# Kernel optimization log

Hardware: AMD Instinct MI355X
Metric: run time of the kernel (lower is better)

The kernel has to match this reference:

```python
import jax, jax.numpy as jnp
import numpy as np
import math

D_MODEL = 256
D_STATE = 64
B, L = 16, 4096
OUT_DIM = 2 * D_MODEL  # bidirectional


def s4d_kernel(log_dt, log_A_real, A_imag, C, L):
    # dt: [d], A: [d, n], C: [d, n, 2]
    dt = jnp.exp(log_dt)
    Cc = C[..., 0] + 1j * C[..., 1]
    A = -jnp.exp(log_A_real) + 1j * A_imag
    dtA = A * dt[:, None]                                   # [d, n]
    Cc = Cc * (jnp.exp(dtA) - 1.0) / (A + 1e-8)
    vand = jnp.exp(dtA[:, :, None] * jnp.arange(L))          # [d, n, L] complex
    K = 2.0 * jnp.einsum('dn,dnl->dl', Cc, vand).real        # [d, L]
    return K


def fft_conv(u, k, L):
    # u: [B, d, L], k: [d, L]; causal conv via zero-padded FFT
    kf = jnp.fft.rfft(k, n=2 * L)
    uf = jnp.fft.rfft(u, n=2 * L)
    return jnp.fft.irfft(uf * kf, n=2 * L)[..., :L]


def setup_inputs() -> dict:
    key = jax.random.key(0)
    ks = jax.random.split(key, 8)
    n = D_STATE // 2

    def kernel_params(k):
        log_dt = jnp.linspace(math.log(0.001), math.log(0.1), D_MODEL)
        log_A_real = jnp.tile(jnp.log(jnp.linspace(0.1, 0.9, n)), (D_MODEL, 1))
        A_imag = jnp.tile(jnp.linspace(0.0, math.pi, n), (D_MODEL, 1))
        C = jax.random.normal(k, (D_MODEL, n, 2)) / math.sqrt(D_STATE)
        return log_dt, log_A_real, A_imag, C

    log_dt_fw, log_A_real_fw, A_imag_fw, C_fw = kernel_params(ks[0])
    log_dt_bw, log_A_real_bw, A_imag_bw, C_bw = kernel_params(ks[1])

    return {
        'x': jax.random.normal(ks[2], (B, L, D_MODEL), dtype=jnp.float32),
        'log_dt_fw': log_dt_fw, 'log_A_real_fw': log_A_real_fw,
        'A_imag_fw': A_imag_fw, 'C_fw': C_fw,
        'log_dt_bw': log_dt_bw, 'log_A_real_bw': log_A_real_bw,
        'A_imag_bw': A_imag_bw, 'C_bw': C_bw,
        'Dskip': jax.random.normal(ks[3], (D_MODEL,)) * 0.01,
        'conv_w': jax.random.normal(ks[4], (2 * OUT_DIM, OUT_DIM)) / math.sqrt(OUT_DIM),
        'conv_b': jnp.zeros((2 * OUT_DIM,)),
        'ln_gamma': jnp.ones((OUT_DIM,)),
        'ln_beta': jnp.zeros((OUT_DIM,)),
    }


def reference(x, log_dt_fw, log_A_real_fw, A_imag_fw, C_fw,
              log_dt_bw, log_A_real_bw, A_imag_bw, C_bw,
              Dskip, conv_w, conv_b, ln_gamma, ln_beta):
    Bsz, Ln, H = x.shape
    u = jnp.swapaxes(x, 1, 2)                                # [B, H, L]

    k_fw = s4d_kernel(log_dt_fw, log_A_real_fw, A_imag_fw, C_fw, Ln)
    y_fw = fft_conv(u, k_fw, Ln) + u * Dskip[:, None]

    u_bw = jnp.flip(u, axis=-1)
    k_bw = s4d_kernel(log_dt_bw, log_A_real_bw, A_imag_bw, C_bw, Ln)
    y_bw = fft_conv(u_bw, k_bw, Ln) + u_bw * Dskip[:, None]
    y_bw = jnp.flip(y_bw, axis=-1)

    y = jnp.concatenate([y_fw, y_bw], axis=1)                # [B, 2H, L]
    y = jax.nn.gelu(y, approximate=False)
    # pointwise conv1d (kernel_size=1): channels 2H -> 4H
    y = jnp.einsum('oc,bcl->bol', conv_w, y) + conv_b[None, :, None]
    a, b = jnp.split(y, 2, axis=1)                           # GLU over channel dim
    y = a * jax.nn.sigmoid(b)                                # [B, 2H, L]
    y = jnp.swapaxes(y, 1, 2)                                # [B, L, 2H]
    # residual skipped: y.shape[-1] (2H) != x.shape[-1] (H)
    mu = jnp.mean(y, axis=-1, keepdims=True)
    var = jnp.var(y, axis=-1, keepdims=True)
    y = (y - mu) * jax.lax.rsqrt(var + 1e-5) * ln_gamma + ln_beta
    return y
```

## Files before the change

### kernel.cpp

```cpp
#include <hip/hip_runtime.h>
#include <hip/hip_bf16.h>
#include <cstdint>
#include <cstddef>

typedef __hip_bfloat16 bf16;
typedef __attribute__((ext_vector_type(8))) short short8;
typedef __attribute__((ext_vector_type(4))) float floatx4;
typedef __attribute__((ext_vector_type(16))) float floatx16;
typedef __attribute__((ext_vector_type(8))) _Float16 half8;

#define Bsz 16
#define Lseq 4096
#define Hd 256
#define NM 32
#define NCH 16
#define TCH 256
#define Mtot (Bsz*Lseq)

__device__ __forceinline__ float gelu_tanh(float y) {
  float y2 = y * y;
  float q = fmaf(0.044715f, y2, 1.0f);
  float a = 1.5957691216057308f * y * q;
  float e = __expf(-a);
  return y * __frcp_rn(1.0f + e);
}

__global__ __launch_bounds__(64) void k_prep(
    const float* __restrict__ ldt_fw, const float* __restrict__ lar_fw,
    const float* __restrict__ ai_fw,  const float* __restrict__ C_fw,
    const float* __restrict__ ldt_bw, const float* __restrict__ lar_bw,
    const float* __restrict__ ai_bw,  const float* __restrict__ C_bw,
    _Float16* __restrict__ Vm, _Float16* __restrict__ P,
    _Float16* __restrict__ KK, float* __restrict__ wtb) {
  const int d = blockIdx.x, dir = blockIdx.y;
  const int lane = threadIdx.x;
  const int n = lane & 31;
  const bool active = lane < 32;
  const float* ldt = dir ? ldt_bw : ldt_fw;
  const float* lar = dir ? lar_bw : lar_fw;
  const float* ai  = dir ? ai_bw  : ai_fw;
  const float* C   = dir ? C_bw   : C_fw;

  float dt = expf(ldt[d]);
  float Ar = -expf(lar[d * NM + n]);
  float Ai = ai[d * NM + n];
  float c0 = C[(d * NM + n) * 2 + 0];
  float c1 = C[(d * NM + n) * 2 + 1];

  float er = expf(Ar * dt);
  float sn, cs;
  sincosf(Ai * dt, &sn, &cs);
  float wr = er * cs, wi = er * sn;
  float nr = wr - 1.f, ni = wi;
  float tr_ = c0 * nr - c1 * ni;
  float ti  = c0 * ni + c1 * nr;
  float dr = Ar + 1e-8f, di = Ai;
  float inv = 1.f / (dr * dr + di * di);
  float Cr = 2.f * (tr_ * dr + ti * di) * inv;
  float Ci = 2.f * (ti * dr - tr_ * di) * inv;
  float erT = expf(256.f * Ar * dt);
  float snT, csT;
  sincosf(256.f * Ai * dt, &snT, &csT);
  if (active) {
    wtb[(dir * 256 + d) * 64 + 2 * n]     = erT * csT;
    wtb[(dir * 256 + d) * 64 + 2 * n + 1] = erT * snT;
  }
  _Float16* kk = KK + (dir * 256 + d) * 512;
  for (int i = lane; i < 512; i += 64) kk[i] = (_Float16)0.f;
  __syncthreads();

  _Float16* vm = Vm + (size_t)(dir * 256 + d) * 64 * 256;
  _Float16* pp = P  + (size_t)(dir * 256 + d) * 256 * 64;
  float pr = 1.f, pi = 0.f;
  for (int j = 0; j <= 256; ++j) {
    float kc = active ? (Cr * pr - Ci * pi) : 0.f;
#pragma unroll
    for (int off = 32; off > 0; off >>= 1) kc += __shfl_xor(kc, off);
    if (lane == 0 && j <= 255) {
      int i = dir ? (255 + j) : (255 - j);
      kk[i] = (_Float16)kc;
    }
    if (active) {
      if (j <= 255) {
        int tv = dir ? j : (255 - j);
        vm[(2 * n) * 256 + tv]     = (_Float16)pr;
        vm[(2 * n + 1) * 256 + tv] = (_Float16)pi;
      }
      if (j >= 1) {
        int t = dir ? (256 - j) : (j - 1);
        float cwr = Cr * pr - Ci * pi;
        float cwi = Cr * pi + Ci * pr;
        pp[t * 64 + 2 * n]     = (_Float16)cwr;
        pp[t * 64 + 2 * n + 1] = (_Float16)(-cwi);
      }
    }
    float npr = pr * wr - pi * wi;
    float npi = pr * wi + pi * wr;
    pr = npr; pi = npi;
  }
}

__global__ __launch_bounds__(256) void k_wconv(
    const float* __restrict__ W, bf16* __restrict__ Wb, int n) {
  int i = blockIdx.x * 256 + threadIdx.x;
  if (i < n) Wb[i] = __float2bfloat16(W[i]);
}

__global__ __launch_bounds__(256) void k_tr(
    const float* __restrict__ x, _Float16* __restrict__ x16) {
  __shared__ __align__(16) _Float16 t16[64][72];
  const int m0 = blockIdx.x * 64, d0 = blockIdx.y * 64;
  const int tid = threadIdx.x;
  {
    int li = tid >> 2, dq = (tid & 3) * 16;
    const float* src = x + (size_t)(m0 + li) * 256 + d0 + dq;
    float4 v0 = ((const float4*)src)[0];
    float4 v1 = ((const float4*)src)[1];
    float4 v2 = ((const float4*)src)[2];
    float4 v3 = ((const float4*)src)[3];
    half8 h0, h1;
    h0[0]=(_Float16)v0.x; h0[1]=(_Float16)v0.y; h0[2]=(_Float16)v0.z; h0[3]=(_Float16)v0.w;
    h0[4]=(_Float16)v1.x; h0[5]=(_Float16)v1.y; h0[6]=(_Float16)v1.z; h0[7]=(_Float16)v1.w;
    h1[0]=(_Float16)v2.x; h1[1]=(_Float16)v2.y; h1[2]=(_Float16)v2.z; h1[3]=(_Float16)v2.w;
    h1[4]=(_Float16)v3.x; h1[5]=(_Float16)v3.y; h1[6]=(_Float16)v3.z; h1[7]=(_Float16)v3.w;
    *(half8*)&t16[li][dq] = h0;
    *(half8*)&t16[li][dq + 8] = h1;
  }
  __syncthreads();
  {
    int dj = tid >> 2, lq = (tid & 3) * 16;
    half8 o0, o1;
#pragma unroll
    for (int i = 0; i < 8; ++i) {
      o0[i] = t16[lq + i][dj];
      o1[i] = t16[lq + 8 + i][dj];
    }
    _Float16* dst = x16 + (size_t)(d0 + dj) * 65536 + m0 + lq;
    ((half8*)dst)[0] = o0;
    ((half8*)dst)[1] = o1;
  }
}

__global__ __launch_bounds__(256) void k_mm1(
    const _Float16* __restrict__ x16, const _Float16* __restrict__ Vm,
    float* __restrict__ Sloc) {
  const int d = blockIdx.x, dir = blockIdx.y;
  const int tid = threadIdx.x, lane = tid & 63, wv = tid >> 6;
  __shared__ __align__(16) _Float16 ub[256][24];
  floatx16 acc[2][2];
#pragma unroll
  for (int a = 0; a < 2; ++a)
#pragma unroll
    for (int b = 0; b < 2; ++b)
#pragma unroll
      for (int i = 0; i < 16; ++i) acc[a][b][i] = 0.f;

  const _Float16* vmp = Vm + (size_t)(dir * 256 + d) * 64 * 256;
  const int arow = lane & 31, ak = (lane >> 5) * 8;
  const int colb = wv * 64;

  for (int ks = 0; ks < 16; ++ks) {
    const int tau0 = ks * 16;
    __syncthreads();
    {
      int col = tid;
      int b = col >> 4, c = col & 15;
      const _Float16* up = x16 + (size_t)d * 65536 + b * 4096 + c * 256 + tau0;
      ((int4*)&ub[col][0])[0] = ((const int4*)up)[0];
      ((int4*)&ub[col][0])[1] = ((const int4*)up)[1];
    }
    __syncthreads();
    half8 a0 = *(const half8*)(vmp + (size_t)(0 * 32 + arow) * 256 + tau0 + ak);
    half8 a1 = *(const half8*)(vmp + (size_t)(1 * 32 + arow) * 256 + tau0 + ak);
    half8 b0 = *(const half8*)&ub[colb + arow][ak];
    half8 b1 = *(const half8*)&ub[colb + 32 + arow][ak];
    acc[0][0] = __builtin_amdgcn_mfma_f32_32x32x16_f16(a0, b0, acc[0][0], 0, 0, 0);
    acc[0][1] = __builtin_amdgcn_mfma_f32_32x32x16_f16(a0, b1, acc[0][1], 0, 0, 0);
    acc[1][0] = __builtin_amdgcn_mfma_f32_32x32x16_f16(a1, b0, acc[1][0], 0, 0, 0);
    acc[1][1] = __builtin_amdgcn_mfma_f32_32x32x16_f16(a1, b1, acc[1][1], 0, 0, 0);
  }
  const int hi = lane >> 5;
#pragma unroll
  for (int rt = 0; rt < 2; ++rt)
#pragma unroll
    for (int ct = 0; ct < 2; ++ct) {
      int coll = colb + ct * 32 + (lane & 31);
      int b = coll >> 4, c = coll & 15;
      float* sp = Sloc + ((((size_t)(b * 2 + dir)) * 16 + c) * 256 + d) * 64;
#pragma unroll
      for (int r = 0; r < 16; r += 2) {
        int n2 = (r & 3) + 8 * (r >> 2) + 4 * hi + rt * 32;
        float2 v;
        v.x = acc[rt][ct][r];
        v.y = acc[rt][ct][r + 1];
        *(float2*)(sp + n2) = v;
      }
    }
}

__global__ __launch_bounds__(256) void k_scan2(
    const float* __restrict__ wtb, float* __restrict__ S) {
  const int b = blockIdx.x, dir = blockIdx.y;
  const int d = blockIdx.z * 64 + (threadIdx.x >> 2), h = threadIdx.x & 3;
  const int nbase = h * 8;
  float wTr[8], wTi[8], sr[8], si[8];
  const float* wt = wtb + (dir * 256 + d) * 64;
#pragma unroll
  for (int n = 0; n < 8; ++n) {
    wTr[n] = wt[2 * (nbase + n)];
    wTi[n] = wt[2 * (nbase + n) + 1];
    sr[n] = 0.f; si[n] = 0.f;
  }
  for (int cc = 0; cc < NCH; ++cc) {
    int c = dir ? (NCH - 1 - cc) : cc;
    float* p = S + ((((size_t)(b * 2 + dir)) * 16 + c) * 256 + d) * 64;
#pragma unroll
    for (int n = 0; n < 8; ++n) {
      int n2 = 2 * (nbase + n);
      float lr = p[n2], li = p[n2 + 1];
      p[n2] = sr[n]; p[n2 + 1] = si[n];
      float t0  = fmaf(wTr[n], sr[n], lr);
      float nsr = fmaf(-wTi[n], si[n], t0);
      float nsi = fmaf(wTr[n], si[n], li);
      nsi = fmaf(wTi[n], sr[n], nsi);
      sr[n] = nsr; si[n] = nsi;
    }
  }
}

__global__ __launch_bounds__(512) void k_mm2(
    const _Float16* __restrict__ x16, const _Float16* __restrict__ KK,
    const _Float16* __restrict__ P, const float* __restrict__ Sstart,
    const float* __restrict__ Dskip, bf16* __restrict__ ActT) {
  const int d = blockIdx.x, dir = blockIdx.y;
  const int tid = threadIdx.x, lane = tid & 63, wv = tid >> 6;
  __shared__ __align__(16) _Float16 ub[64][272];
  __shared__ __align__(16) _Float16 sb[64][72];
  __shared__ __align__(16) _Float16 kks[8][520];

  {
    const _Float16* kg = KK + (dir * 256 + d) * 512;
#pragma unroll
    for (int rr = 0; rr < 8; ++rr)
      for (int xx = tid; xx < 520; xx += 512) {
        int s = xx + rr;
        kks[rr][xx] = (s < 512) ? kg[s] : (_Float16)0.f;
      }
  }
  const float Dk = Dskip[d];
  const int t = wv * 32 + (lane & 31);
  const int hi = lane >> 5;
  const int r_sh = (255 - t) & 7;
  const _Float16* pp = P + (size_t)(dir * 256 + d) * 256 * 64 + (size_t)t * 64;

  for (int cb = 0; cb < 4; ++cb) {
    __syncthreads();
    {
      int col = tid >> 3, part = tid & 7;
      int coll = cb * 64 + col;
      int b = coll >> 4, c = coll & 15;
      const _Float16* up = x16 + (size_t)d * 65536 + b * 4096 + c * 256 + part * 32;
      ((int4*)&ub[col][part * 32])[0] = ((const int4*)up)[0];
      ((int4*)&ub[col][part * 32])[1] = ((const int4*)up)[1];
      ((int4*)&ub[col][part * 32])[2] = ((const int4*)up)[2];
      ((int4*)&ub[col][part * 32])[3] = ((const int4*)up)[3];
    }
    {
      int col = tid >> 3, part = tid & 7;
      int coll = cb * 64 + col;
      int b = coll >> 4, c = coll & 15;
      const float* sp = Sstart + ((((size_t)(b * 2 + dir)) * 16 + c) * 256 + d) * 64 + part * 8;
      float4 f0 = ((const float4*)sp)[0];
      float4 f1 = ((const float4*)sp)[1];
      half8 hv;
      hv[0]=(_Float16)f0.x; hv[1]=(_Float16)f0.y; hv[2]=(_Float16)f0.z; hv[3]=(_Float16)f0.w;
      hv[4]=(_Float16)f1.x; hv[5]=(_Float16)f1.y; hv[6]=(_Float16)f1.z; hv[7]=(_Float16)f1.w;
      *(half8*)&sb[col][part * 8] = hv;
    }
    __syncthreads();

    floatx16 acc0, acc1;
#pragma unroll
    for (int i = 0; i < 16; ++i) { acc0[i] = 0.f; acc1[i] = 0.f; }

#pragma unroll
    for (int ks = 0; ks < 16; ++ks) {
      int i0 = 255 - t + ks * 16 + hi * 8;
      half8 af = *(const half8*)&kks[r_sh][i0 - r_sh];
      half8 b0 = *(const half8*)&ub[(lane & 31)][ks * 16 + hi * 8];
      half8 b1 = *(const half8*)&ub[32 + (lane & 31)][ks * 16 + hi * 8];
      acc0 = __builtin_amdgcn_mfma_f32_32x32x16_f16(af, b0, acc0, 0, 0, 0);
      acc1 = __builtin_amdgcn_mfma_f32_32x32x16_f16(af, b1, acc1, 0, 0, 0);
    }
#pragma unroll
    for (int ks = 0; ks < 4; ++ks) {
      half8 af = *(const half8*)(pp + ks * 16 + hi * 8);
      half8 b0 = *(const half8*)&sb[(lane & 31)][ks * 16 + hi * 8];
      half8 b1 = *(const half8*)&sb[32 + (lane & 31)][ks * 16 + hi * 8];
      acc0 = __builtin_amdgcn_mfma_f32_32x32x16_f16(af, b0, acc0, 0, 0, 0);
      acc1 = __builtin_amdgcn_mfma_f32_32x32x16_f16(af, b1, acc1, 0, 0, 0);
    }
#pragma unroll
    for (int ct = 0; ct < 2; ++ct) {
      int coll = cb * 64 + ct * 32 + (lane & 31);
      int b = coll >> 4, c = coll & 15;
      bf16* op = ActT + (size_t)(dir * 256 + d) * 65536 + b * 4096 + c * 256;
      int ucol = ct * 32 + (lane & 31);
#pragma unroll
      for (int r = 0; r < 16; r += 2) {
        int tt = (r & 3) + 8 * (r >> 2) + 4 * hi + wv * 32;
        float a0 = (ct ? acc1[r] : acc0[r]);
        float a1 = (ct ? acc1[r + 1] : acc0[r + 1]);
        float u0 = (float)ub[ucol][tt];
        float u1 = (float)ub[ucol][tt + 1];
        float g0 = gelu_tanh(fmaf(u0, Dk, a0));
        float g1 = gelu_tanh(fmaf(u1, Dk, a1));
        bf16 h0 = __float2bfloat16(g0);
        bf16 h1 = __float2bfloat16(g1);
        unsigned pk = (unsigned)*(unsigned short*)&h0 |
                      ((unsigned)*(unsigned short*)&h1 << 16);
        *(unsigned*)(op + tt) = pk;
      }
    }
  }
}

__global__ __launch_bounds__(256) void k_tr2(
    const bf16* __restrict__ AT, bf16* __restrict__ A) {
  __shared__ __align__(16) short tl[64][72];
  const int m0 = blockIdx.x * 64, ch0 = blockIdx.y * 64;
  const int tid = threadIdx.x;
  {
    int chi = tid >> 2, mq = (tid & 3) * 16;
    const short* src = (const short*)AT + (size_t)(ch0 + chi) * 65536 + m0 + mq;
    *(int4*)&tl[chi][mq] = ((const int4*)src)[0];
    *(int4*)&tl[chi][mq + 8] = ((const int4*)src)[1];
  }
  __syncthreads();
  {
    int mi = tid >> 2, chq = (tid & 3) * 16;
    short8 s0, s1;
#pragma unroll
    for (int i = 0; i < 8; ++i) {
      s0[i] = tl[chq + i][mi];
      s1[i] = tl[chq + 8 + i][mi];
    }
    short* dst = (short*)A + (size_t)(m0 + mi) * 512 + ch0 + chq;
    ((short8*)dst)[0] = s0;
    ((short8*)dst)[1] = s1;
  }
}

#define LDK 40
__global__ __launch_bounds__(256, 4) void k_gemm(
    const bf16* __restrict__ Act, const bf16* __restrict__ W,
    const float* __restrict__ bias, float* __restrict__ z) {
  __shared__ __align__(16) short As[128 * LDK];
  __shared__ __align__(16) short Bas[64 * LDK];
  __shared__ __align__(16) short Bgs[64 * LDK];
  const int id = blockIdx.x;
  const int x = id & 7, nj = (id >> 3) & 7, g = id >> 6;
  const int bi = g * 8 + x;
  const int tid = threadIdx.x, lane = tid & 63, wv = tid >> 6;
  const int wm = (wv & 1) * 64, wn = (wv >> 1) * 32;
  const int M0 = bi * 128, N0 = nj * 64;
  floatx4 acc_a[4][2], acc_g[4][2];
#pragma unroll
  for (int i = 0; i < 4; ++i)
#pragma unroll
    for (int j = 0; j < 2; ++j) {
      acc_a[i][j] = (floatx4){0.f, 0.f, 0.f, 0.f};
      acc_g[i][j] = (floatx4){0.f, 0.f, 0.f, 0.f};
    }
  const int row2 = tid >> 2;
  const int kc = (tid & 3) * 8;
  const int fr = lane & 15, fk = (lane >> 4) * 8;

  const bf16* pa0 = Act + (size_t)(M0 + row2) * 512 + kc;
  const bf16* pa1 = Act + (size_t)(M0 + row2 + 64) * 512 + kc;
  const bf16* pba = W + (size_t)(N0 + row2) * 512 + kc;
  const bf16* pbg = W + (size_t)(512 + N0 + row2) * 512 + kc;

  *(int4*)&As[row2 * LDK + kc]        = *(const int4*)pa0;
  *(int4*)&As[(row2 + 64) * LDK + kc] = *(const int4*)pa1;
  *(int4*)&Bas[row2 * LDK + kc]       = *(const int4*)pba;
  *(int4*)&Bgs[row2 * LDK + kc]       = *(const int4*)pbg;

  for (int kb = 0; kb < 512; kb += 32) {
    __syncthreads();
    short8 af[4], bfa[2], bfg[2];
#pragma unroll
    for (int i = 0; i < 4; ++i) af[i]  = *(const short8*)&As[(wm + 16 * i + fr) * LDK + fk];
#pragma unroll
    for (int j = 0; j < 2; ++j) bfa[j] = *(const short8*)&Bas[(wn + 16 * j + fr) * LDK + fk];
#pragma unroll
    for (int j = 0; j < 2; ++j) bfg[j] = *(const short8*)&Bgs[(wn + 16 * j + fr) * LDK + fk];
    int4 ga0, ga1, gb, gg;
    const bool more = (kb + 32) < 512;
    if (more) {
      ga0 = *(const int4*)(pa0 + kb + 32);
      ga1 = *(const int4*)(pa1 + kb + 32);
      gb  = *(const int4*)(pba + kb + 32);
      gg  = *(const int4*)(pbg + kb + 32);
    }
#pragma unroll
    for (int i = 0; i < 4; ++i)
#pragma unroll
      for (int j = 0; j < 2; ++j) {
        acc_a[i][j] = __builtin_amdgcn_mfma_f32_16x16x32_bf16(af[i], bfa[j], acc_a[i][j], 0, 0, 0);
        acc_g[i][j] = __builtin_amdgcn_mfma_f32_16x16x32_bf16(af[i], bfg[j], acc_g[i][j], 0, 0, 0);
      }
    __syncthreads();
    if (more) {
      *(int4*)&As[row2 * LDK + kc]        = ga0;
      *(int4*)&As[(row2 + 64) * LDK + kc] = ga1;
      *(int4*)&Bas[row2 * LDK + kc]       = gb;
      *(int4*)&Bgs[row2 * LDK + kc]       = gg;
    }
  }
  const int col = lane & 15, rquad = (lane >> 4) * 4;
#pragma unroll
  for (int j = 0; j < 2; ++j) {
    int o = N0 + wn + 16 * j + col;
    float ba = bias[o];
    float bg = bias[512 + o];
#pragma unroll
    for (int i = 0; i < 4; ++i) {
      int mbase = M0 + wm + 16 * i + rquad;
#pragma unroll
      for (int rg = 0; rg < 4; ++rg) {
        float a = acc_a[i][j][rg] + ba;
        float g = acc_g[i][j][rg] + bg;
        float zv = a * __frcp_rn(1.f + __expf(-g));
        z[(size_t)(mbase + rg) * 512 + o] = zv;
      }
    }
  }
}

__global__ __launch_bounds__(256) void k_ln(
    float* __restrict__ z, const float* __restrict__ gamma,
    const float* __restrict__ beta) {
  const int m = blockIdx.x * 4 + (threadIdx.x >> 6);
  const int lane = threadIdx.x & 63;
  float* zp = z + (size_t)m * 512;
  float v[8], s = 0.f, sq = 0.f;
#pragma unroll
  for (int j = 0; j < 8; ++j) {
    v[j] = zp[j * 64 + lane];
    s += v[j];
    sq = fmaf(v[j], v[j], sq);
  }
#pragma unroll
  for (int off = 32; off > 0; off >>= 1) {
    s += __shfl_xor(s, off);
    sq += __shfl_xor(sq, off);
  }
  float mean = s * (1.f / 512.f);
  float var = fmaf(-mean, mean, sq * (1.f / 512.f));
  float inv = rsqrtf(var + 1e-5f);
#pragma unroll
  for (int j = 0; j < 8; ++j) {
    int cidx = j * 64 + lane;
    float g = gamma[cidx], be = beta[cidx];
    zp[cidx] = fmaf((v[j] - mean) * inv, g, be);
  }
}

extern "C" void kernel_launch(void* const* d_in, const int* in_sizes, int n_in,
                              void* d_out, int out_size, void* d_ws, size_t ws_size,
                              hipStream_t stream) {
  const float* x      = (const float*)d_in[0];
  const float* ldt_fw = (const float*)d_in[1];
  const float* lar_fw = (const float*)d_in[2];
  const float* ai_fw  = (const float*)d_in[3];
  const float* C_fw   = (const float*)d_in[4];
  const float* ldt_bw = (const float*)d_in[5];
  const float* lar_bw = (const float*)d_in[6];
  const float* ai_bw  = (const float*)d_in[7];
  const float* C_bw   = (const float*)d_in[8];
  const float* Dskip  = (const float*)d_in[9];
  const float* W      = (const float*)d_in[10];
  const float* bias   = (const float*)d_in[11];
  const float* gamma  = (const float*)d_in[12];
  const float* beta   = (const float*)d_in[13];
  float* out = (float*)d_out;

  char* wsb = (char*)d_ws;
  bf16*     ActT  = (bf16*)wsb;
  float*    SlocT = (float*)(wsb + 67108864u);
  _Float16* x16   = (_Float16*)(wsb + 100663296u);
  _Float16* Vm    = (_Float16*)(wsb + 134217728u);
  _Float16* P     = (_Float16*)(wsb + 150994944u);
  _Float16* KK    = (_Float16*)(wsb + 167772160u);
  float*    wtb   = (float*)(wsb + 168296448u);
  bf16*     Wb    = (bf16*)(wsb + 168427520u);
  bf16*     Act   = (bf16*)(wsb + 67108864u);

  k_prep<<<dim3(256, 2), dim3(64), 0, stream>>>(
      ldt_fw, lar_fw, ai_fw, C_fw, ldt_bw, lar_bw, ai_bw, C_bw, Vm, P, KK, wtb);
  k_wconv<<<dim3(2048), dim3(256), 0, stream>>>(W, Wb, 1024 * 512);
  k_tr<<<dim3(Mtot / 64, 4), dim3(256), 0, stream>>>(x, x16);
  k_mm1<<<dim3(256, 2), dim3(256), 0, stream>>>(x16, Vm, SlocT);
  k_scan2<<<dim3(Bsz, 2, 4), dim3(256), 0, stream>>>(wtb, SlocT);
  k_mm2<<<dim3(256, 2), dim3(512), 0, stream>>>(x16, KK, P, SlocT, Dskip, ActT);
  k_tr2<<<dim3(Mtot / 64, 8), dim3(256), 0, stream>>>(ActT, Act);
  k_gemm<<<dim3(4096), dim3(256), 0, stream>>>(Act, Wb, bias, out);
  k_ln<<<dim3(Mtot / 4), dim3(256), 0, stream>>>(out, gamma, beta);
}
```

Before: 516.1 us.

## Load GEMM MFMA fragments directly from global memory, dropping LDS staging

The pointwise-conv GEMM no longer stages A and B tiles in shared memory with double-buffered register prefetch and barriers. Each wave now loads its MFMA operand fragments straight from global memory, and the K loop is unrolled by four. This removes the LDS traffic and the __syncthreads calls, but data that several waves share in a block is now fetched redundantly through L1/L2. The per-lane loads are also less coalesced: 16-byte reads strided by a full row.

```diff
diff --git a/kernel.cpp b/kernel.cpp
--- a/kernel.cpp
+++ b/kernel.cpp
@@ -351,13 +351,9 @@
   }
 }
 
-#define LDK 40
 __global__ __launch_bounds__(256, 4) void k_gemm(
     const bf16* __restrict__ Act, const bf16* __restrict__ W,
     const float* __restrict__ bias, float* __restrict__ z) {
-  __shared__ __align__(16) short As[128 * LDK];
-  __shared__ __align__(16) short Bas[64 * LDK];
-  __shared__ __align__(16) short Bgs[64 * LDK];
   const int id = blockIdx.x;
   const int x = id & 7, nj = (id >> 3) & 7, g = id >> 6;
   const int bi = g * 8 + x;
@@ -372,36 +368,22 @@
       acc_a[i][j] = (floatx4){0.f, 0.f, 0.f, 0.f};
       acc_g[i][j] = (floatx4){0.f, 0.f, 0.f, 0.f};
     }
-  const int row2 = tid >> 2;
-  const int kc = (tid & 3) * 8;
   const int fr = lane & 15, fk = (lane >> 4) * 8;
 
-  const bf16* pa0 = Act + (size_t)(M0 + row2) * 512 + kc;
-  const bf16* pa1 = Act + (size_t)(M0 + row2 + 64) * 512 + kc;
-  const bf16* pba = W + (size_t)(N0 + row2) * 512 + kc;
-  const bf16* pbg = W + (size_t)(512 + N0 + row2) * 512 + kc;
-
-  *(int4*)&As[row2 * LDK + kc]        = *(const int4*)pa0;
-  *(int4*)&As[(row2 + 64) * LDK + kc] = *(const int4*)pa1;
-  *(int4*)&Bas[row2 * LDK + kc]       = *(const int4*)pba;
-  *(int4*)&Bgs[row2 * LDK + kc]       = *(const int4*)pbg;
-
+  const bf16* pA  = Act + (size_t)(M0 + wm + fr) * 512 + fk;
+  const bf16* pBa = W + (size_t)(N0 + wn + fr) * 512 + fk;
+  const bf16* pBg = W + (size_t)(512 + N0 + wn + fr) * 512 + fk;
+
+#pragma unroll 4
   for (int kb = 0; kb < 512; kb += 32) {
-    __syncthreads();
     short8 af[4], bfa[2], bfg[2];
 #pragma unroll
-    for (int i = 0; i < 4; ++i) af[i]  = *(const short8*)&As[(wm + 16 * i + fr) * LDK + fk];
-#pragma unroll
-    for (int j = 0; j < 2; ++j) bfa[j] = *(const short8*)&Bas[(wn + 16 * j + fr) * LDK + fk];
-#pragma unroll
-    for (int j = 0; j < 2; ++j) bfg[j] = *(const short8*)&Bgs[(wn + 16 * j + fr) * LDK + fk];
-    int4 ga0, ga1, gb, gg;
-    const bool more = (kb + 32) < 512;
-    if (more) {
-      ga0 = *(const int4*)(pa0 + kb + 32);
-      ga1 = *(const int4*)(pa1 + kb + 32);
-      gb  = *(const int4*)(pba + kb + 32);
-      gg  = *(const int4*)(pbg + kb + 32);
+    for (int i = 0; i < 4; ++i)
+      af[i] = *(const short8*)(pA + (size_t)(16 * i) * 512 + kb);
+#pragma unroll
+    for (int j = 0; j < 2; ++j) {
+      bfa[j] = *(const short8*)(pBa + (size_t)(16 * j) * 512 + kb);
+      bfg[j] = *(const short8*)(pBg + (size_t)(16 * j) * 512 + kb);
     }
 #pragma unroll
     for (int i = 0; i < 4; ++i)
@@ -410,13 +392,6 @@
         acc_a[i][j] = __builtin_amdgcn_mfma_f32_16x16x32_bf16(af[i], bfa[j], acc_a[i][j], 0, 0, 0);
         acc_g[i][j] = __builtin_amdgcn_mfma_f32_16x16x32_bf16(af[i], bfg[j], acc_g[i][j], 0, 0, 0);
       }
-    __syncthreads();
-    if (more) {
-      *(int4*)&As[row2 * LDK + kc]        = ga0;
-      *(int4*)&As[(row2 + 64) * LDK + kc] = ga1;
-      *(int4*)&Bas[row2 * LDK + kc]       = gb;
-      *(int4*)&Bgs[row2 * LDK + kc]       = gg;
-    }
   }
   const int col = lane & 15, rquad = (lane >> 4) * 4;
 #pragma unroll
```

Result: slower. 669.2 us (+29.7%).
